# Performance work log

Measured on AMD Instinct MI355X. Metric: run time of the kernel, lower is better.

The kernel has to match this reference:

```python
import jax, jax.numpy as jnp
import numpy as np

N = 100000   # nodes
E = 1600000  # edges
EPS = 1e-5


def _gcn_conv(x, W, b, src, dst, dinv):
    # PyG GCNConv with self-loops: out_i = sum_{j->i} d_j^-1/2 d_i^-1/2 (x_j W) + d_i^-1 (x_i W) + b
    h = x @ W                                   # [N, out]
    coef = dinv[src] * dinv[dst]                # [E]
    agg = jax.ops.segment_sum(h[src] * coef[:, None], dst, num_segments=N)
    agg = agg + h * (dinv * dinv)[:, None]      # self-loop term
    return agg + b


def _bn_eval(x, gamma, beta, mean, var):
    return (x - mean) * jax.lax.rsqrt(var + EPS) * gamma + beta


def setup_inputs() -> dict:
    key = jax.random.key(0)
    ks = jax.random.split(key, 8)
    F_IN, H, C = 128, 256, 32
    inp = {
        "x": jax.random.normal(ks[0], (N, F_IN), dtype=jnp.float32),
        "edge_index": jax.random.randint(ks[1], (2, E), 0, N, dtype=jnp.int64),
        # layer 1
        "W1": jax.random.normal(ks[2], (F_IN, H), dtype=jnp.float32) / np.sqrt(F_IN),
        "b1": jnp.zeros((H,), jnp.float32),
        "g1": jnp.ones((H,), jnp.float32),
        "be1": jnp.zeros((H,), jnp.float32),
        "m1": jax.random.normal(ks[3], (H,), dtype=jnp.float32) * 0.1,
        "v1": jnp.ones((H,), jnp.float32),
        # layer 2
        "W2": jax.random.normal(ks[4], (H, H), dtype=jnp.float32) / np.sqrt(H),
        "b2": jnp.zeros((H,), jnp.float32),
        "g2": jnp.ones((H,), jnp.float32),
        "be2": jnp.zeros((H,), jnp.float32),
        "m2": jax.random.normal(ks[5], (H,), dtype=jnp.float32) * 0.1,
        "v2": jnp.ones((H,), jnp.float32),
        # layer 3
        "W3": jax.random.normal(ks[6], (H, C), dtype=jnp.float32) / np.sqrt(H),
        "b3": jnp.zeros((C,), jnp.float32),
    }
    return inp


def reference(x, edge_index, W1, b1, g1, be1, m1, v1,
              W2, b2, g2, be2, m2, v2, W3, b3):
    src, dst = edge_index[0], edge_index[1]
    # degree with self-loops: in-degree + 1
    deg = jnp.zeros((N,), x.dtype).at[dst].add(1.0) + 1.0
    dinv = jax.lax.rsqrt(deg)

    h = _gcn_conv(x, W1, b1, src, dst, dinv)
    h = jax.nn.relu(_bn_eval(h, g1, be1, m1, v1))
    h = _gcn_conv(h, W2, b2, src, dst, dinv)
    h = jax.nn.relu(_bn_eval(h, g2, be2, m2, v2))
    h = _gcn_conv(h, W3, b3, src, dst, dinv)
    return jax.nn.sigmoid(h)
```

## Files before the change

kernel.cpp:

```cpp
#include <hip/hip_runtime.h>
#include <math.h>

typedef unsigned short u16;
typedef unsigned char u8;
typedef unsigned int u32;
typedef __attribute__((ext_vector_type(8))) __bf16 bfx8;
typedef __attribute__((ext_vector_type(4))) float f32x4;
typedef __attribute__((ext_vector_type(2))) float f32x2;
typedef __attribute__((ext_vector_type(8))) unsigned short us8;
typedef __attribute__((ext_vector_type(4))) unsigned short us4;

__device__ inline float bf2f(u16 u) {
    union { unsigned int i; float f; } v;
    v.i = ((unsigned int)u) << 16;
    return v.f;
}
__device__ inline u16 f2bf(float f) {
    union { float f; unsigned int i; } v;
    v.f = f;
    unsigned int b = v.i;
    return (u16)((b + 0x7FFFu + ((b >> 16) & 1u)) >> 16);
}
__device__ inline u32 bits_of(float f) {
    union { float f; u32 i; } v; v.f = f; return v.i;
}
__device__ inline u32 pkbf(float a, float b) {
    return (bits_of(a) >> 16) | (bits_of(b) & 0xffff0000u);
}
__device__ inline void dec4(u32 d, u32& lo, u32& hi) {
    f32x2 a = __builtin_amdgcn_cvt_pk_f32_fp8(d, false);
    f32x2 b = __builtin_amdgcn_cvt_pk_f32_fp8(d, true);
    lo = pkbf(a[0], a[1]);
    hi = pkbf(b[0], b[1]);
}


__global__ __launch_bounds__(256) void k_hist(const int* __restrict__ ei,
                                              u32* __restrict__ cnt_pb,
                                              int E, int NB, int NBLK) {
    __shared__ u32 h[256];
    int blk = blockIdx.x, tid = threadIdx.x;
    h[tid] = 0;
    __syncthreads();
    int eend = min(E, (blk + 1) * 2048);
    for (int e = blk * 2048 + tid; e < eend; e += 256) {
        int d = ei[E + e];
        atomicAdd(&h[d >> 9], 1u);
    }
    __syncthreads();
    if (tid < NB) cnt_pb[(size_t)tid * NBLK + blk] = h[tid];
}

__global__ __launch_bounds__(1024) void k_scanb(const u32* __restrict__ cnt_pb,
                                                u32* __restrict__ bases_pb,
                                                u32* __restrict__ bkt_tot,
                                                int NBLK) {
    __shared__ u32 lds[1024];
    int b = blockIdx.x, t = threadIdx.x;
    u32 v = (t < NBLK) ? cnt_pb[(size_t)b * NBLK + t] : 0u;
    lds[t] = v;
    __syncthreads();
    for (int off = 1; off < 1024; off <<= 1) {
        u32 x = lds[t];
        u32 y = (t >= off) ? lds[t - off] : 0u;
        __syncthreads();
        lds[t] = x + y;
        __syncthreads();
    }
    if (t < NBLK) bases_pb[(size_t)b * NBLK + t] = lds[t] - v;
    if (t == NBLK - 1) bkt_tot[b] = lds[t];
}

__global__ __launch_bounds__(256) void k_scant(const u32* __restrict__ bkt_tot,
                                               u32* __restrict__ bkt_base,
                                               int* __restrict__ row_ptr,
                                               int NB, int N, int E) {
    __shared__ u32 lds[256];
    int t = threadIdx.x;
    u32 v = (t < NB) ? bkt_tot[t] : 0u;
    lds[t] = v;
    __syncthreads();
    for (int off = 1; off < 256; off <<= 1) {
        u32 x = lds[t];
        u32 y = (t >= off) ? lds[t - off] : 0u;
        __syncthreads();
        lds[t] = x + y;
        __syncthreads();
    }
    if (t < NB) bkt_base[t] = lds[t] - v;
    if (t == 0) row_ptr[N] = E;
}

__global__ __launch_bounds__(256) void k_scatter2(const int* __restrict__ ei,
                                                  const u32* __restrict__ bases_pb,
                                                  const u32* __restrict__ bkt_base,
                                                  u32* __restrict__ bkt_edges,
                                                  int E, int NB, int NBLK) {
    __shared__ u32 cur[256];
    __shared__ u32 bb[256];
    int blk = blockIdx.x, tid = threadIdx.x;
    if (tid < NB) {
        cur[tid] = bases_pb[(size_t)tid * NBLK + blk];
        bb[tid] = bkt_base[tid];
    }
    __syncthreads();
    int eend = min(E, (blk + 1) * 2048);
    for (int e = blk * 2048 + tid; e < eend; e += 256) {
        int s = ei[e];
        int d = ei[E + e];
        int b = d >> 9;
        int dl = d & 511;
        u32 off = atomicAdd(&cur[b], 1u);
        bkt_edges[bb[b] + off] = (u32)s | ((u32)dl << 17);
    }
}

__global__ __launch_bounds__(512) void k_bucket(const u32* __restrict__ bkt_edges,
                                                const u32* __restrict__ bkt_base,
                                                const u32* __restrict__ bkt_tot,
                                                int* __restrict__ row_ptr,
                                                float* __restrict__ dinv,
                                                int* __restrict__ csr_src,
                                                int N) {
    __shared__ u32 lcnt[512];
    __shared__ u32 lscan[512];
    int b = blockIdx.x, t = threadIdx.x;
    int node0 = b << 9;
    int es = (int)bkt_base[b];
    int ce = (int)bkt_tot[b];
    lcnt[t] = 0;
    __syncthreads();
    for (int i = t; i < ce; i += 512) {
        u32 p = bkt_edges[es + i];
        atomicAdd(&lcnt[p >> 17], 1u);
    }
    __syncthreads();
    lscan[t] = lcnt[t];
    __syncthreads();
    for (int off = 1; off < 512; off <<= 1) {
        u32 x = lscan[t];
        u32 y = (t >= off) ? lscan[t - off] : 0u;
        __syncthreads();
        lscan[t] = x + y;
        __syncthreads();
    }
    u32 excl = lscan[t] - lcnt[t];
    int node = node0 + t;
    if (node < N) {
        row_ptr[node] = es + (int)excl;
        dinv[node] = rsqrtf((float)lcnt[t] + 1.0f);
    }
    __syncthreads();
    lscan[t] = excl;
    __syncthreads();
    for (int i = t; i < ce; i += 512) {
        u32 p = bkt_edges[es + i];
        int dl = (int)(p >> 17);
        int src = (int)(p & 0x1FFFFu);
        u32 pos = atomicAdd(&lscan[dl], 1u);
        csr_src[es + pos] = src;
    }
}


__global__ void k_bnfold(const float* __restrict__ b, const float* __restrict__ g,
                         const float* __restrict__ be, const float* __restrict__ m,
                         const float* __restrict__ v, float* __restrict__ s,
                         float* __restrict__ t, int H) {
    int i = blockIdx.x * blockDim.x + threadIdx.x;
    if (i < H) {
        float sc = g[i] * rsqrtf(v[i] + 1e-5f);
        s[i] = sc;
        t[i] = (b[i] - m[i]) * sc + be[i];
    }
}

__global__ void k_w2bf(const float* __restrict__ W, u16* __restrict__ Wt, int K, int F) {
    int i = blockIdx.x * blockDim.x + threadIdx.x;
    if (i < K * F) {
        int k = i / F, f = i % F;
        Wt[(size_t)f * K + k] = f2bf(W[i]);
    }
}

__global__ void k_x2f8(const float* __restrict__ x, u8* __restrict__ xq,
                       const float* __restrict__ dinv, int n4) {
    int i = blockIdx.x * blockDim.x + threadIdx.x;
    if (i < n4) {
        float d = dinv[i >> 5];
        float4 v = *(const float4*)(x + (size_t)i * 4);
        unsigned int pk = 0;
        pk = __builtin_amdgcn_cvt_pk_fp8_f32(v.x * d, v.y * d, pk, false);
        pk = __builtin_amdgcn_cvt_pk_fp8_f32(v.z * d, v.w * d, pk, true);
        *(unsigned int*)(xq + (size_t)i * 4) = pk;
    }
}

template<int K, int FT, int MODE, bool AFP8, int MINW>
__global__ __launch_bounds__(256, MINW) void g_mfma_lds(
    const void* __restrict__ Av, const u16* __restrict__ Wt,
    void* __restrict__ Cv, int M, int Ftot,
    const float* __restrict__ s, const float* __restrict__ t,
    const float* __restrict__ dinv, int nTiles)
{
    constexpr int BK  = 128;
    constexpr int SA  = BK + 8;
    constexpr int NH  = K / BK;
    constexpr int NKH = BK / 32;
    constexpr int NF  = FT / 16;
    constexpr int EB  = (MODE == 3) ? 1 : 2;
    constexpr int SCB = FT * EB + 16;
    constexpr int EBa = AFP8 ? 1 : 2;
    constexpr int CR  = (BK * EBa) / 16;
    constexpr int LIT = (64 * CR) / 256;

    __shared__ u16 Asmem[2][64 * SA];
    __shared__ u8  Cs8[64 * SCB];

    const u8* Ab = (const u8*)Av;
    int tid = threadIdx.x;
    int w = tid >> 6, l = tid & 63;
    int lr = l & 15, koff8 = (l >> 4) * 8;
    int col0 = blockIdx.y * FT;

    bfx8 bfr[NH][NKH][NF];
    {
        const u16* wp = Wt + (size_t)(col0 + lr) * K + koff8;
        #pragma unroll
        for (int h = 0; h < NH; ++h)
            #pragma unroll
            for (int kk = 0; kk < NKH; ++kk)
                #pragma unroll
                for (int c = 0; c < NF; ++c)
                    bfr[h][kk][c] = *(const bfx8*)(wp + (size_t)c * 16 * K + h * BK + kk * 32);
    }

    int myT = (blockIdx.x < nTiles) ? ((nTiles - 1 - (int)blockIdx.x) / (int)gridDim.x + 1) : 0;
    int NM = myT * NH;
    if (NM == 0) return;

    f32x4 acc[NF];
    #pragma unroll
    for (int c = 0; c < NF; ++c) acc[c] = (f32x4){0.f, 0.f, 0.f, 0.f};

    uint4 rga[LIT];

    auto loadA = [&](int r0, int hh) {
        #pragma unroll
        for (int j = 0; j < LIT; ++j) {
            int cid = j * 256 + tid;
            int row = cid / CR, ch = cid % CR;
            int gr = r0 + row; if (gr > M - 1) gr = M - 1;
            rga[j] = *(const uint4*)(Ab + (size_t)gr * K * EBa + (size_t)hh * BK * EBa + ch * 16);
        }
    };
    auto writeA = [&](int buf) {
        #pragma unroll
        for (int j = 0; j < LIT; ++j) {
            int cid = j * 256 + tid;
            int row = cid / CR, ch = cid % CR;
            if (!AFP8) {
                *(uint4*)&Asmem[buf][row * SA + ch * 8] = rga[j];
            } else {
                u32 w0, w1, w2, w3, w4, w5, w6, w7;
                dec4(rga[j].x, w0, w1);
                dec4(rga[j].y, w2, w3);
                dec4(rga[j].z, w4, w5);
                dec4(rga[j].w, w6, w7);
                uint4 lo4; lo4.x = w0; lo4.y = w1; lo4.z = w2; lo4.w = w3;
                uint4 hi4; hi4.x = w4; hi4.y = w5; hi4.z = w6; hi4.w = w7;
                *(uint4*)&Asmem[buf][row * SA + ch * 16] = lo4;
                *(uint4*)&Asmem[buf][row * SA + ch * 16 + 8] = hi4;
            }
        }
    };

    loadA(blockIdx.x * 64, 0);
    writeA(0);
    if (NM > 1) {
        constexpr int gt1 = 1 / NH, h1 = 1 % NH;
        loadA((blockIdx.x + gt1 * gridDim.x) * 64, h1);
    }
    __syncthreads();

    int cur = 0, gm = 0;
    for (int ti = 0; ti < myT; ++ti) {
        int row0g = (blockIdx.x + ti * gridDim.x) * 64;
        #pragma unroll
        for (int h = 0; h < NH; ++h) {
            const u16* ab = &Asmem[cur][0];
            #pragma unroll
            for (int kk = 0; kk < NKH; ++kk) {
                bfx8 af = *(const bfx8*)(ab + (w * 16 + lr) * SA + koff8 + kk * 32);
                #pragma unroll
                for (int c = 0; c < NF; ++c)
                    acc[c] = __builtin_amdgcn_mfma_f32_16x16x32_bf16(af, bfr[h][kk][c], acc[c], 0, 0, 0);
            }
            if (h == NH - 1) {
                int orow = w * 16 + (l >> 4) * 4;
                float dr[4];
                #pragma unroll
                for (int r = 0; r < 4; ++r) {
                    int grow = row0g + orow + r;
                    dr[r] = (MODE == 2) ? 1.f : ((grow < M) ? dinv[grow] : 0.f);
                }
                #pragma unroll
                for (int c = 0; c < NF; ++c) {
                    int gc = col0 + c * 16 + lr;
                    float sc = (MODE == 2) ? 0.f : s[gc];
                    float tc = (MODE == 2) ? 0.f : t[gc];
                    #pragma unroll
                    for (int r = 0; r < 4; ++r) {
                        float v = acc[c][r];
                        if (MODE != 2) v = fmaxf(v * sc + tc, 0.f) * dr[r];
                        if (MODE == 3) {
                            int enc = __builtin_amdgcn_cvt_pk_fp8_f32(v, v, 0, false);
                            Cs8[(orow + r) * SCB + (c * 16 + lr)] = (u8)(enc & 0xff);
                        } else {
                            *(u16*)&Cs8[(orow + r) * SCB + (c * 16 + lr) * 2] = f2bf(v);
                        }
                    }
                    acc[c] = (f32x4){0.f, 0.f, 0.f, 0.f};
                }
            }
            __syncthreads();
            if (gm + 1 < NM) writeA(cur ^ 1);
            if (h == NH - 1) {
                constexpr int CPR = (FT * EB) / 16;
                constexpr int CPT = (64 * CPR) / 256;
                u8* C8 = (u8*)Cv;
                #pragma unroll
                for (int j = 0; j < CPT; ++j) {
                    int cid = j * 256 + tid;
                    int crow = cid / CPR;
                    int cb = (cid % CPR) * 16;
                    int grow = row0g + crow;
                    if (grow < M) {
                        us8 vv = *(const us8*)&Cs8[crow * SCB + cb];
                        *(us8*)(C8 + (size_t)grow * Ftot * EB + (size_t)col0 * EB + cb) = vv;
                    }
                }
            }
            if (gm + 2 < NM) {
                int g2 = gm + 2;
                int gt2 = g2 / NH, h2 = g2 % NH;
                loadA((blockIdx.x + gt2 * gridDim.x) * 64, h2);
            }
            __syncthreads();
            cur ^= 1; ++gm;
        }
    }
}

__global__ __launch_bounds__(256) void agg_x(const u8* __restrict__ in,
                                             u8* __restrict__ outp,
                                             const int* __restrict__ row_ptr,
                                             const int* __restrict__ csr_src,
                                             const float* __restrict__ dinv,
                                             int nnodes) {
    int tid = threadIdx.x;
    int wv = tid >> 6, lane = tid & 63;
    int half = lane >> 5, l32 = lane & 31;
    int node = (blockIdx.x * 4 + wv) * 2 + half;
    if (node >= nnodes) return;
    int off = l32 * 4;
    const u8* bp = in + off;
    float a0, a1, a2, a3;
    {
        unsigned int q = *(const unsigned int*)(in + (size_t)node * 128 + off);
        f32x2 p;
        p = __builtin_amdgcn_cvt_pk_f32_fp8(q, false); a0 = p[0]; a1 = p[1];
        p = __builtin_amdgcn_cvt_pk_f32_fp8(q, true);  a2 = p[0]; a3 = p[1];
    }
    int e = row_ptr[node], e1 = row_ptr[node + 1];
    for (; e + 8 <= e1; e += 8) {
        int sx[8];
        #pragma unroll
        for (int q = 0; q < 8; ++q) sx[q] = csr_src[e + q];
        unsigned int vv[8];
        #pragma unroll
        for (int q = 0; q < 8; ++q) vv[q] = *(const unsigned int*)(bp + (size_t)sx[q] * 128);
        #pragma unroll
        for (int q = 0; q < 8; ++q) {
            f32x2 p;
            p = __builtin_amdgcn_cvt_pk_f32_fp8(vv[q], false); a0 += p[0]; a1 += p[1];
            p = __builtin_amdgcn_cvt_pk_f32_fp8(vv[q], true);  a2 += p[0]; a3 += p[1];
        }
    }
    for (; e < e1; ++e) {
        int s0 = csr_src[e];
        unsigned int v0 = *(const unsigned int*)(bp + (size_t)s0 * 128);
        f32x2 p;
        p = __builtin_amdgcn_cvt_pk_f32_fp8(v0, false); a0 += p[0]; a1 += p[1];
        p = __builtin_amdgcn_cvt_pk_f32_fp8(v0, true);  a2 += p[0]; a3 += p[1];
    }
    float d = dinv[node];
    u32 pk = 0;
    pk = __builtin_amdgcn_cvt_pk_fp8_f32(a0 * d, a1 * d, pk, false);
    pk = __builtin_amdgcn_cvt_pk_fp8_f32(a2 * d, a3 * d, pk, true);
    *(u32*)(outp + (size_t)node * 128 + off) = pk;
}

__global__ __launch_bounds__(256) void agg_h(const u8* __restrict__ in,
                                             u8* __restrict__ outp,
                                             const int* __restrict__ row_ptr,
                                             const int* __restrict__ csr_src,
                                             const float* __restrict__ dinv,
                                             int nnodes) {
    int tid = threadIdx.x;
    int wv = tid >> 6, lane = tid & 63;
    int half = lane >> 5, l32 = lane & 31;
    int node = (blockIdx.x * 4 + wv) * 2 + half;
    if (node >= nnodes) return;
    int off = l32 * 8;
    const u8* bp = in + off;
    float acc[8];
    {
        uint2 q = *(const uint2*)(in + (size_t)node * 256 + off);
        f32x2 p;
        p = __builtin_amdgcn_cvt_pk_f32_fp8(q.x, false); acc[0] = p[0]; acc[1] = p[1];
        p = __builtin_amdgcn_cvt_pk_f32_fp8(q.x, true);  acc[2] = p[0]; acc[3] = p[1];
        p = __builtin_amdgcn_cvt_pk_f32_fp8(q.y, false); acc[4] = p[0]; acc[5] = p[1];
        p = __builtin_amdgcn_cvt_pk_f32_fp8(q.y, true);  acc[6] = p[0]; acc[7] = p[1];
    }
    int e = row_ptr[node], e1 = row_ptr[node + 1];
    for (; e + 8 <= e1; e += 8) {
        int sx[8];
        #pragma unroll
        for (int q = 0; q < 8; ++q) sx[q] = csr_src[e + q];
        uint2 vv[8];
        #pragma unroll
        for (int q = 0; q < 8; ++q) vv[q] = *(const uint2*)(bp + (size_t)sx[q] * 256);
        #pragma unroll
        for (int q = 0; q < 8; ++q) {
            f32x2 p;
            p = __builtin_amdgcn_cvt_pk_f32_fp8(vv[q].x, false); acc[0] += p[0]; acc[1] += p[1];
            p = __builtin_amdgcn_cvt_pk_f32_fp8(vv[q].x, true);  acc[2] += p[0]; acc[3] += p[1];
            p = __builtin_amdgcn_cvt_pk_f32_fp8(vv[q].y, false); acc[4] += p[0]; acc[5] += p[1];
            p = __builtin_amdgcn_cvt_pk_f32_fp8(vv[q].y, true);  acc[6] += p[0]; acc[7] += p[1];
        }
    }
    for (; e < e1; ++e) {
        int s0 = csr_src[e];
        uint2 v0 = *(const uint2*)(bp + (size_t)s0 * 256);
        f32x2 p;
        p = __builtin_amdgcn_cvt_pk_f32_fp8(v0.x, false); acc[0] += p[0]; acc[1] += p[1];
        p = __builtin_amdgcn_cvt_pk_f32_fp8(v0.x, true);  acc[2] += p[0]; acc[3] += p[1];
        p = __builtin_amdgcn_cvt_pk_f32_fp8(v0.y, false); acc[4] += p[0]; acc[5] += p[1];
        p = __builtin_amdgcn_cvt_pk_f32_fp8(v0.y, true);  acc[6] += p[0]; acc[7] += p[1];
    }
    float d = dinv[node];
    u32 w0 = 0, w1 = 0;
    w0 = __builtin_amdgcn_cvt_pk_fp8_f32(acc[0] * d, acc[1] * d, w0, false);
    w0 = __builtin_amdgcn_cvt_pk_fp8_f32(acc[2] * d, acc[3] * d, w0, true);
    w1 = __builtin_amdgcn_cvt_pk_fp8_f32(acc[4] * d, acc[5] * d, w1, false);
    w1 = __builtin_amdgcn_cvt_pk_fp8_f32(acc[6] * d, acc[7] * d, w1, true);
    uint2 o; o.x = w0; o.y = w1;
    *(uint2*)(outp + (size_t)node * 256 + off) = o;
}

__global__ __launch_bounds__(256) void agg32_sig(const u16* __restrict__ z,
                                                 float* __restrict__ out,
                                                 const int* __restrict__ row_ptr,
                                                 const int* __restrict__ csr_src,
                                                 const float* __restrict__ dinv,
                                                 const float* __restrict__ b3,
                                                 int nnodes) {
    int tid = threadIdx.x;
    int wv = tid >> 6, lane = tid & 63;
    int half = lane >> 5, l32 = lane & 31;
    int node = (blockIdx.x * 4 + wv) * 2 + half;
    if (node >= nnodes) return;
    float acc = bf2f(z[(size_t)node * 32 + l32]);
    int e = row_ptr[node], e1 = row_ptr[node + 1];
    for (; e + 4 <= e1; e += 4) {
        int s0 = csr_src[e], s1 = csr_src[e + 1], s2 = csr_src[e + 2], s3 = csr_src[e + 3];
        float z0 = bf2f(z[(size_t)s0 * 32 + l32]);
        float z1 = bf2f(z[(size_t)s1 * 32 + l32]);
        float z2 = bf2f(z[(size_t)s2 * 32 + l32]);
        float z3v = bf2f(z[(size_t)s3 * 32 + l32]);
        acc += z0 + z1 + z2 + z3v;
    }
    for (; e < e1; ++e) {
        acc += bf2f(z[(size_t)csr_src[e] * 32 + l32]);
    }
    acc = acc * dinv[node] + b3[l32];
    out[(size_t)node * 32 + l32] = 1.f / (1.f + expf(-acc));
}


extern "C" void kernel_launch(void* const* d_in, const int* in_sizes, int n_in,
                              void* d_out, int out_size, void* d_ws, size_t ws_size,
                              hipStream_t stream) {
    const float* x  = (const float*)d_in[0];
    const int*   ei = (const int*)d_in[1];
    const float* W1 = (const float*)d_in[2];
    const float* b1 = (const float*)d_in[3];
    const float* g1 = (const float*)d_in[4];
    const float* be1 = (const float*)d_in[5];
    const float* m1 = (const float*)d_in[6];
    const float* v1 = (const float*)d_in[7];
    const float* W2 = (const float*)d_in[8];
    const float* b2 = (const float*)d_in[9];
    const float* g2 = (const float*)d_in[10];
    const float* be2 = (const float*)d_in[11];
    const float* m2 = (const float*)d_in[12];
    const float* v2 = (const float*)d_in[13];
    const float* W3 = (const float*)d_in[14];
    const float* b3 = (const float*)d_in[15];
    float* out = (float*)d_out;

    const int N = in_sizes[0] / 128;
    const int E = in_sizes[1] / 2;

    const int NB = (N + 511) >> 9;
    const int NBLK = (E + 2047) / 2048;

    char* w = (char*)d_ws;
    auto alloc = [&](size_t bytes) -> void* {
        void* p = (void*)w;
        w += (bytes + 255) & ~(size_t)255;
        return p;
    };
    int* row_ptr   = (int*)alloc((size_t)(N + 1) * 4);
    float* dinv    = (float*)alloc((size_t)N * 4);
    u32* cnt_pb    = (u32*)alloc((size_t)NB * NBLK * 4);
    u32* bases_pb  = (u32*)alloc((size_t)NB * NBLK * 4);
    u32* bkt_tot   = (u32*)alloc((size_t)NB * 4);
    u32* bkt_base  = (u32*)alloc((size_t)NB * 4);
    u32* bkt_edges = (u32*)alloc((size_t)E * 4);
    float* s1 = (float*)alloc(256 * 4);
    float* t1 = (float*)alloc(256 * 4);
    float* s2 = (float*)alloc(256 * 4);
    float* t2 = (float*)alloc(256 * 4);
    u16* Wt1 = (u16*)alloc((size_t)128 * 256 * 2);
    u16* Wt2 = (u16*)alloc((size_t)256 * 256 * 2);
    u16* Wt3 = (u16*)alloc((size_t)256 * 32 * 2);
    int* csr_src = (int*)alloc((size_t)E * 4);
    u8*  xq   = (u8*)alloc((size_t)N * 128);
    u8*  xa   = (u8*)alloc((size_t)N * 128);
    u8*  h1q  = (u8*)alloc((size_t)N * 256);
    u8*  h1a  = (u8*)alloc((size_t)N * 256);
    u8*  h2q  = (u8*)alloc((size_t)N * 256);
    u16* z3 = (u16*)xq;

    int nT = (N + 63) / 64;
    int gagg = (N + 7) / 8;

    k_hist<<<NBLK, 256, 0, stream>>>(ei, cnt_pb, E, NB, NBLK);
    k_scanb<<<NB, 1024, 0, stream>>>(cnt_pb, bases_pb, bkt_tot, NBLK);
    k_scant<<<1, 256, 0, stream>>>(bkt_tot, bkt_base, row_ptr, NB, N, E);
    k_scatter2<<<NBLK, 256, 0, stream>>>(ei, bases_pb, bkt_base, bkt_edges, E, NB, NBLK);
    k_bucket<<<NB, 512, 0, stream>>>(bkt_edges, bkt_base, bkt_tot, row_ptr, dinv, csr_src, N);

    k_bnfold<<<1, 256, 0, stream>>>(b1, g1, be1, m1, v1, s1, t1, 256);
    k_bnfold<<<1, 256, 0, stream>>>(b2, g2, be2, m2, v2, s2, t2, 256);
    k_w2bf<<<(128 * 256 + 255) / 256, 256, 0, stream>>>(W1, Wt1, 128, 256);
    k_w2bf<<<(256 * 256 + 255) / 256, 256, 0, stream>>>(W2, Wt2, 256, 256);
    k_w2bf<<<(256 * 32 + 255) / 256, 256, 0, stream>>>(W3, Wt3, 256, 32);
    k_x2f8<<<(N * 128 / 4 + 255) / 256, 256, 0, stream>>>(x, xq, dinv, N * 128 / 4);

    agg_x<<<gagg, 256, 0, stream>>>(xq, xa, row_ptr, csr_src, dinv, N);
    g_mfma_lds<128, 64, 3, true, 2><<<dim3(128, 4), 256, 0, stream>>>(
        (const void*)xa, Wt1, (void*)h1q, N, 256, s1, t1, dinv, nT);

    agg_h<<<gagg, 256, 0, stream>>>(h1q, h1a, row_ptr, csr_src, dinv, N);
    g_mfma_lds<256, 64, 3, true, 2><<<dim3(128, 4), 256, 0, stream>>>(
        (const void*)h1a, Wt2, (void*)h2q, N, 256, s2, t2, dinv, nT);

    g_mfma_lds<256, 32, 2, true, 2><<<dim3(512, 1), 256, 0, stream>>>(
        (const void*)h2q, Wt3, (void*)z3, N, 32, (const float*)nullptr,
        (const float*)nullptr, (const float*)nullptr, nT);
    agg32_sig<<<gagg, 256, 0, stream>>>(z3, out, row_ptr, csr_src, dinv, b3, N);
}
```

Before: 282.5 us.

## Merge prep kernels, fold bucket scan into consumers, store layer-3 output as fp8

Removes the standalone bucket-total scan kernel by redoing the small 256-entry scan inside both the scatter and bucket kernels. Merges the weight conversion, BN folding and x-to-fp8 kernels into one prep launch. Switches the layer-3 GEMM output from bf16 to fp8 (new MODE 4) and rewrites the final aggregation so 8 lanes each gather 4 fp8 values per node. This cuts launch count and gather bytes in the last layer, at the cost of redundant scans and reduced output precision.

```diff
diff --git a/kernel.cpp b/kernel.cpp
--- a/kernel.cpp
+++ b/kernel.cpp
@@ -71,38 +71,28 @@
     if (t == NBLK - 1) bkt_tot[b] = lds[t];
 }
 
-__global__ __launch_bounds__(256) void k_scant(const u32* __restrict__ bkt_tot,
-                                               u32* __restrict__ bkt_base,
-                                               int* __restrict__ row_ptr,
-                                               int NB, int N, int E) {
-    __shared__ u32 lds[256];
-    int t = threadIdx.x;
-    u32 v = (t < NB) ? bkt_tot[t] : 0u;
-    lds[t] = v;
-    __syncthreads();
-    for (int off = 1; off < 256; off <<= 1) {
-        u32 x = lds[t];
-        u32 y = (t >= off) ? lds[t - off] : 0u;
-        __syncthreads();
-        lds[t] = x + y;
-        __syncthreads();
-    }
-    if (t < NB) bkt_base[t] = lds[t] - v;
-    if (t == 0) row_ptr[N] = E;
-}
-
 __global__ __launch_bounds__(256) void k_scatter2(const int* __restrict__ ei,
                                                   const u32* __restrict__ bases_pb,
-                                                  const u32* __restrict__ bkt_base,
+                                                  const u32* __restrict__ bkt_tot,
                                                   u32* __restrict__ bkt_edges,
                                                   int E, int NB, int NBLK) {
     __shared__ u32 cur[256];
     __shared__ u32 bb[256];
     int blk = blockIdx.x, tid = threadIdx.x;
-    if (tid < NB) {
-        cur[tid] = bases_pb[(size_t)tid * NBLK + blk];
-        bb[tid] = bkt_base[tid];
-    }
+    u32 v = (tid < NB) ? bkt_tot[tid] : 0u;
+    bb[tid] = v;
+    __syncthreads();
+    for (int off = 1; off < 256; off <<= 1) {
+        u32 x = bb[tid];
+        u32 y = (tid >= off) ? bb[tid - off] : 0u;
+        __syncthreads();
+        bb[tid] = x + y;
+        __syncthreads();
+    }
+    u32 excl = bb[tid] - v;
+    __syncthreads();
+    bb[tid] = excl;
+    if (tid < NB) cur[tid] = bases_pb[(size_t)tid * NBLK + blk];
     __syncthreads();
     int eend = min(E, (blk + 1) * 2048);
     for (int e = blk * 2048 + tid; e < eend; e += 256) {
@@ -116,18 +106,27 @@
 }
 
 __global__ __launch_bounds__(512) void k_bucket(const u32* __restrict__ bkt_edges,
-                                                const u32* __restrict__ bkt_base,
                                                 const u32* __restrict__ bkt_tot,
                                                 int* __restrict__ row_ptr,
                                                 float* __restrict__ dinv,
                                                 int* __restrict__ csr_src,
-                                                int N) {
+                                                int N, int NB, int E) {
+    __shared__ u32 sb[256];
     __shared__ u32 lcnt[512];
     __shared__ u32 lscan[512];
     int b = blockIdx.x, t = threadIdx.x;
+    if (t < 256) sb[t] = (t < NB) ? bkt_tot[t] : 0u;
+    __syncthreads();
+    for (int off = 1; off < 256; off <<= 1) {
+        u32 x = 0, y = 0;
+        if (t < 256) { x = sb[t]; y = (t >= off) ? sb[t - off] : 0u; }
+        __syncthreads();
+        if (t < 256) sb[t] = x + y;
+        __syncthreads();
+    }
+    int ce = (int)bkt_tot[b];
+    int es = (int)sb[b] - ce;
     int node0 = b << 9;
-    int es = (int)bkt_base[b];
-    int ce = (int)bkt_tot[b];
     lcnt[t] = 0;
     __syncthreads();
     for (int i = t; i < ce; i += 512) {
@@ -150,6 +149,7 @@
         row_ptr[node] = es + (int)excl;
         dinv[node] = rsqrtf((float)lcnt[t] + 1.0f);
     }
+    if (b == 0 && t == 0) row_ptr[N] = E;
     __syncthreads();
     lscan[t] = excl;
     __syncthreads();
@@ -162,37 +162,52 @@
     }
 }
 
-
-__global__ void k_bnfold(const float* __restrict__ b, const float* __restrict__ g,
-                         const float* __restrict__ be, const float* __restrict__ m,
-                         const float* __restrict__ v, float* __restrict__ s,
-                         float* __restrict__ t, int H) {
-    int i = blockIdx.x * blockDim.x + threadIdx.x;
-    if (i < H) {
-        float sc = g[i] * rsqrtf(v[i] + 1e-5f);
-        s[i] = sc;
-        t[i] = (b[i] - m[i]) * sc + be[i];
-    }
-}
-
-__global__ void k_w2bf(const float* __restrict__ W, u16* __restrict__ Wt, int K, int F) {
-    int i = blockIdx.x * blockDim.x + threadIdx.x;
-    if (i < K * F) {
-        int k = i / F, f = i % F;
-        Wt[(size_t)f * K + k] = f2bf(W[i]);
-    }
-}
-
-__global__ void k_x2f8(const float* __restrict__ x, u8* __restrict__ xq,
-                       const float* __restrict__ dinv, int n4) {
+__global__ __launch_bounds__(256) void k_prep(
+    const float* __restrict__ x, u8* __restrict__ xq, const float* __restrict__ dinv, int n4,
+    const float* __restrict__ W1, u16* __restrict__ Wt1,
+    const float* __restrict__ W2, u16* __restrict__ Wt2,
+    const float* __restrict__ W3, u16* __restrict__ Wt3,
+    const float* __restrict__ b1, const float* __restrict__ g1, const float* __restrict__ be1,
+    const float* __restrict__ m1, const float* __restrict__ v1,
+    float* __restrict__ s1, float* __restrict__ t1,
+    const float* __restrict__ b2, const float* __restrict__ g2, const float* __restrict__ be2,
+    const float* __restrict__ m2, const float* __restrict__ v2,
+    float* __restrict__ s2, float* __restrict__ t2)
+{
     int i = blockIdx.x * blockDim.x + threadIdx.x;
     if (i < n4) {
         float d = dinv[i >> 5];
         float4 v = *(const float4*)(x + (size_t)i * 4);
-        unsigned int pk = 0;
+        u32 pk = 0;
         pk = __builtin_amdgcn_cvt_pk_fp8_f32(v.x * d, v.y * d, pk, false);
         pk = __builtin_amdgcn_cvt_pk_fp8_f32(v.z * d, v.w * d, pk, true);
-        *(unsigned int*)(xq + (size_t)i * 4) = pk;
+        *(u32*)(xq + (size_t)i * 4) = pk;
+        return;
+    }
+    int j = i - n4;
+    if (j < 128 * 256) {
+        int k = j / 256, f = j % 256;
+        Wt1[(size_t)f * 128 + k] = f2bf(W1[j]);
+    } else if (j < 128 * 256 + 256 * 256) {
+        int j2 = j - 128 * 256;
+        int k = j2 / 256, f = j2 % 256;
+        Wt2[(size_t)f * 256 + k] = f2bf(W2[j2]);
+    } else if (j < 128 * 256 + 256 * 256 + 256 * 32) {
+        int j3 = j - (128 * 256 + 256 * 256);
+        int k = j3 / 32, f = j3 % 32;
+        Wt3[(size_t)f * 256 + k] = f2bf(W3[j3]);
+    } else {
+        int k = j - (128 * 256 + 256 * 256 + 256 * 32);
+        if (k < 256) {
+            float sc = g1[k] * rsqrtf(v1[k] + 1e-5f);
+            s1[k] = sc;
+            t1[k] = (b1[k] - m1[k]) * sc + be1[k];
+        } else if (k < 512) {
+            int kk = k - 256;
+            float sc = g2[kk] * rsqrtf(v2[kk] + 1e-5f);
+            s2[kk] = sc;
+            t2[kk] = (b2[kk] - m2[kk]) * sc + be2[kk];
+        }
     }
 }
 
@@ -203,12 +218,14 @@
     const float* __restrict__ s, const float* __restrict__ t,
     const float* __restrict__ dinv, int nTiles)
 {
+    constexpr bool DOBN = (MODE == 1) || (MODE == 3);
+    constexpr bool CF8  = (MODE >= 3);
     constexpr int BK  = 128;
     constexpr int SA  = BK + 8;
     constexpr int NH  = K / BK;
     constexpr int NKH = BK / 32;
     constexpr int NF  = FT / 16;
-    constexpr int EB  = (MODE == 3) ? 1 : 2;
+    constexpr int EB  = CF8 ? 1 : 2;
     constexpr int SCB = FT * EB + 16;
     constexpr int EBa = AFP8 ? 1 : 2;
     constexpr int CR  = (BK * EBa) / 16;
@@ -302,18 +319,18 @@
                 #pragma unroll
                 for (int r = 0; r < 4; ++r) {
                     int grow = row0g + orow + r;
-                    dr[r] = (MODE == 2) ? 1.f : ((grow < M) ? dinv[grow] : 0.f);
+                    dr[r] = DOBN ? ((grow < M) ? dinv[grow] : 0.f) : 1.f;
                 }
                 #pragma unroll
                 for (int c = 0; c < NF; ++c) {
                     int gc = col0 + c * 16 + lr;
-                    float sc = (MODE == 2) ? 0.f : s[gc];
-                    float tc = (MODE == 2) ? 0.f : t[gc];
+                    float sc = DOBN ? s[gc] : 0.f;
+                    float tc = DOBN ? t[gc] : 0.f;
                     #pragma unroll
                     for (int r = 0; r < 4; ++r) {
                         float v = acc[c][r];
-                        if (MODE != 2) v = fmaxf(v * sc + tc, 0.f) * dr[r];
-                        if (MODE == 3) {
+                        if (DOBN) v = fmaxf(v * sc + tc, 0.f) * dr[r];
+                        if (CF8) {
                             int enc = __builtin_amdgcn_cvt_pk_fp8_f32(v, v, 0, false);
                             Cs8[(orow + r) * SCB + (c * 16 + lr)] = (u8)(enc & 0xff);
                         } else {
@@ -327,17 +344,20 @@
             if (gm + 1 < NM) writeA(cur ^ 1);
             if (h == NH - 1) {
                 constexpr int CPR = (FT * EB) / 16;
-                constexpr int CPT = (64 * CPR) / 256;
+                constexpr int TOT = 64 * CPR;
+                constexpr int CPT = (TOT + 255) / 256;
                 u8* C8 = (u8*)Cv;
                 #pragma unroll
                 for (int j = 0; j < CPT; ++j) {
                     int cid = j * 256 + tid;
-                    int crow = cid / CPR;
-                    int cb = (cid % CPR) * 16;
-                    int grow = row0g + crow;
-                    if (grow < M) {
-                        us8 vv = *(const us8*)&Cs8[crow * SCB + cb];
-                        *(us8*)(C8 + (size_t)grow * Ftot * EB + (size_t)col0 * EB + cb) = vv;
+                    if (cid < TOT) {
+                        int crow = cid / CPR;
+                        int cb = (cid % CPR) * 16;
+                        int grow = row0g + crow;
+                        if (grow < M) {
+                            us8 vv = *(const us8*)&Cs8[crow * SCB + cb];
+                            *(us8*)(C8 + (size_t)grow * Ftot * EB + (size_t)col0 * EB + cb) = vv;
+                        }
                     }
                 }
             }
@@ -367,7 +387,7 @@
     const u8* bp = in + off;
     float a0, a1, a2, a3;
     {
-        unsigned int q = *(const unsigned int*)(in + (size_t)node * 128 + off);
+        u32 q = *(const u32*)(in + (size_t)node * 128 + off);
         f32x2 p;
         p = __builtin_amdgcn_cvt_pk_f32_fp8(q, false); a0 = p[0]; a1 = p[1];
         p = __builtin_amdgcn_cvt_pk_f32_fp8(q, true);  a2 = p[0]; a3 = p[1];
@@ -377,9 +397,9 @@
         int sx[8];
         #pragma unroll
         for (int q = 0; q < 8; ++q) sx[q] = csr_src[e + q];
-        unsigned int vv[8];
-        #pragma unroll
-        for (int q = 0; q < 8; ++q) vv[q] = *(const unsigned int*)(bp + (size_t)sx[q] * 128);
+        u32 vv[8];
+        #pragma unroll
+        for (int q = 0; q < 8; ++q) vv[q] = *(const u32*)(bp + (size_t)sx[q] * 128);
         #pragma unroll
         for (int q = 0; q < 8; ++q) {
             f32x2 p;
@@ -389,7 +409,7 @@
     }
     for (; e < e1; ++e) {
         int s0 = csr_src[e];
-        unsigned int v0 = *(const unsigned int*)(bp + (size_t)s0 * 128);
+        u32 v0 = *(const u32*)(bp + (size_t)s0 * 128);
         f32x2 p;
         p = __builtin_amdgcn_cvt_pk_f32_fp8(v0, false); a0 += p[0]; a1 += p[1];
         p = __builtin_amdgcn_cvt_pk_f32_fp8(v0, true);  a2 += p[0]; a3 += p[1];
@@ -459,7 +479,7 @@
     *(uint2*)(outp + (size_t)node * 256 + off) = o;
 }
 
-__global__ __launch_bounds__(256) void agg32_sig(const u16* __restrict__ z,
+__global__ __launch_bounds__(256) void agg32_sig(const u8* __restrict__ zq,
                                                  float* __restrict__ out,
                                                  const int* __restrict__ row_ptr,
                                                  const int* __restrict__ csr_src,
@@ -467,25 +487,48 @@
                                                  const float* __restrict__ b3,
                                                  int nnodes) {
     int tid = threadIdx.x;
-    int wv = tid >> 6, lane = tid & 63;
-    int half = lane >> 5, l32 = lane & 31;
-    int node = (blockIdx.x * 4 + wv) * 2 + half;
+    int grp = tid >> 3, l8 = tid & 7;
+    int node = blockIdx.x * 32 + grp;
     if (node >= nnodes) return;
-    float acc = bf2f(z[(size_t)node * 32 + l32]);
+    int off = l8 * 4;
+    const u8* bp = zq + off;
+    float a0, a1, a2, a3;
+    {
+        u32 q = *(const u32*)(zq + (size_t)node * 32 + off);
+        f32x2 p;
+        p = __builtin_amdgcn_cvt_pk_f32_fp8(q, false); a0 = p[0]; a1 = p[1];
+        p = __builtin_amdgcn_cvt_pk_f32_fp8(q, true);  a2 = p[0]; a3 = p[1];
+    }
     int e = row_ptr[node], e1 = row_ptr[node + 1];
-    for (; e + 4 <= e1; e += 4) {
-        int s0 = csr_src[e], s1 = csr_src[e + 1], s2 = csr_src[e + 2], s3 = csr_src[e + 3];
-        float z0 = bf2f(z[(size_t)s0 * 32 + l32]);
-        float z1 = bf2f(z[(size_t)s1 * 32 + l32]);
-        float z2 = bf2f(z[(size_t)s2 * 32 + l32]);
-        float z3v = bf2f(z[(size_t)s3 * 32 + l32]);
-        acc += z0 + z1 + z2 + z3v;
+    for (; e + 8 <= e1; e += 8) {
+        int sx[8];
+        #pragma unroll
+        for (int q = 0; q < 8; ++q) sx[q] = csr_src[e + q];
+        u32 vv[8];
+        #pragma unroll
+        for (int q = 0; q < 8; ++q) vv[q] = *(const u32*)(bp + (size_t)sx[q] * 32);
+        #pragma unroll
+        for (int q = 0; q < 8; ++q) {
+            f32x2 p;
+            p = __builtin_amdgcn_cvt_pk_f32_fp8(vv[q], false); a0 += p[0]; a1 += p[1];
+            p = __builtin_amdgcn_cvt_pk_f32_fp8(vv[q], true);  a2 += p[0]; a3 += p[1];
+        }
     }
     for (; e < e1; ++e) {
-        acc += bf2f(z[(size_t)csr_src[e] * 32 + l32]);
-    }
-    acc = acc * dinv[node] + b3[l32];
-    out[(size_t)node * 32 + l32] = 1.f / (1.f + expf(-acc));
+        int s0 = csr_src[e];
+        u32 v0 = *(const u32*)(bp + (size_t)s0 * 32);
+        f32x2 p;
+        p = __builtin_amdgcn_cvt_pk_f32_fp8(v0, false); a0 += p[0]; a1 += p[1];
+        p = __builtin_amdgcn_cvt_pk_f32_fp8(v0, true);  a2 += p[0]; a3 += p[1];
+    }
+    float d = dinv[node];
+    int fb = l8 * 4;
+    float4 o;
+    o.x = 1.f / (1.f + expf(-(a0 * d + b3[fb + 0])));
+    o.y = 1.f / (1.f + expf(-(a1 * d + b3[fb + 1])));
+    o.z = 1.f / (1.f + expf(-(a2 * d + b3[fb + 2])));
+    o.w = 1.f / (1.f + expf(-(a3 * d + b3[fb + 3])));
+    *(float4*)(out + (size_t)node * 32 + fb) = o;
 }
 
 
@@ -527,7 +570,6 @@
     u32* cnt_pb    = (u32*)alloc((size_t)NB * NBLK * 4);
     u32* bases_pb  = (u32*)alloc((size_t)NB * NBLK * 4);
     u32* bkt_tot   = (u32*)alloc((size_t)NB * 4);
-    u32* bkt_base  = (u32*)alloc((size_t)NB * 4);
     u32* bkt_edges = (u32*)alloc((size_t)E * 4);
     float* s1 = (float*)alloc(256 * 4);
     float* t1 = (float*)alloc(256 * 4);
@@ -542,23 +584,21 @@
     u8*  h1q  = (u8*)alloc((size_t)N * 256);
     u8*  h1a  = (u8*)alloc((size_t)N * 256);
     u8*  h2q  = (u8*)alloc((size_t)N * 256);
-    u16* z3 = (u16*)xq;
+    u8*  z3 = xq;
 
     int nT = (N + 63) / 64;
     int gagg = (N + 7) / 8;
+    int n4 = N * 128 / 4;
+    int prepTot = n4 + 128 * 256 + 256 * 256 + 256 * 32 + 512;
 
     k_hist<<<NBLK, 256, 0, stream>>>(ei, cnt_pb, E, NB, NBLK);
     k_scanb<<<NB, 1024, 0, stream>>>(cnt_pb, bases_pb, bkt_tot, NBLK);
-    k_scant<<<1, 256, 0, stream>>>(bkt_tot, bkt_base, row_ptr, NB, N, E);
-    k_scatter2<<<NBLK, 256, 0, stream>>>(ei, bases_pb, bkt_base, bkt_edges, E, NB, NBLK);
-    k_bucket<<<NB, 512, 0, stream>>>(bkt_edges, bkt_base, bkt_tot, row_ptr, dinv, csr_src, N);
-
-    k_bnfold<<<1, 256, 0, stream>>>(b1, g1, be1, m1, v1, s1, t1, 256);
-    k_bnfold<<<1, 256, 0, stream>>>(b2, g2, be2, m2, v2, s2, t2, 256);
-    k_w2bf<<<(128 * 256 + 255) / 256, 256, 0, stream>>>(W1, Wt1, 128, 256);
-    k_w2bf<<<(256 * 256 + 255) / 256, 256, 0, stream>>>(W2, Wt2, 256, 256);
-    k_w2bf<<<(256 * 32 + 255) / 256, 256, 0, stream>>>(W3, Wt3, 256, 32);
-    k_x2f8<<<(N * 128 / 4 + 255) / 256, 256, 0, stream>>>(x, xq, dinv, N * 128 / 4);
+    k_scatter2<<<NBLK, 256, 0, stream>>>(ei, bases_pb, bkt_tot, bkt_edges, E, NB, NBLK);
+    k_bucket<<<NB, 512, 0, stream>>>(bkt_edges, bkt_tot, row_ptr, dinv, csr_src, N, NB, E);
+
+    k_prep<<<(prepTot + 255) / 256, 256, 0, stream>>>(
+        x, xq, dinv, n4, W1, Wt1, W2, Wt2, W3, Wt3,
+        b1, g1, be1, m1, v1, s1, t1, b2, g2, be2, m2, v2, s2, t2);
 
     agg_x<<<gagg, 256, 0, stream>>>(xq, xa, row_ptr, csr_src, dinv, N);
     g_mfma_lds<128, 64, 3, true, 2><<<dim3(128, 4), 256, 0, stream>>>(
@@ -568,8 +608,8 @@
     g_mfma_lds<256, 64, 3, true, 2><<<dim3(128, 4), 256, 0, stream>>>(
         (const void*)h1a, Wt2, (void*)h2q, N, 256, s2, t2, dinv, nT);
 
-    g_mfma_lds<256, 32, 2, true, 2><<<dim3(512, 1), 256, 0, stream>>>(
+    g_mfma_lds<256, 32, 4, true, 2><<<dim3(512, 1), 256, 0, stream>>>(
         (const void*)h2q, Wt3, (void*)z3, N, 32, (const float*)nullptr,
         (const float*)nullptr, (const float*)nullptr, nT);
-    agg32_sig<<<gagg, 256, 0, stream>>>(z3, out, row_ptr, csr_src, dinv, b3, N);
-}
+    agg32_sig<<<(N + 31) / 32, 256, 0, stream>>>(z3, out, row_ptr, csr_src, dinv, b3, N);
+}
```

Result: faster. 251.6 us (-10.9%).
